# Performance work log

Hardware: AMD Instinct MI355X
Metric: run time of the kernel (lower is better)

Reference implementation:

```python
import jax, jax.numpy as jnp
import numpy as np

N = 50000   # nodes
E = 600000  # edges
D = 128     # in_feats
H = 128     # n_hidden
C = 47      # n_classes


def setup_inputs() -> dict:
    key = jax.random.key(0)
    ks = jax.random.split(key, 12)
    x = jax.random.normal(ks[0], (N, D), dtype=jnp.float32)
    src = jax.random.randint(ks[1], (E,), 0, N, dtype=jnp.int32)
    dst = jax.random.randint(ks[2], (E,), 0, N, dtype=jnp.int32)
    def lin(k, fi, fo):
        s = 1.0 / np.sqrt(fi)
        return jax.random.uniform(k, (fi, fo), jnp.float32, -s, s)
    return {
        "x": x, "src": src, "dst": dst,
        "W_self0": lin(ks[3], D, H), "W_neigh0": lin(ks[4], D, H), "b0": jnp.zeros((H,), jnp.float32),
        "W_self1": lin(ks[5], H, H), "W_neigh1": lin(ks[6], H, H), "b1": jnp.zeros((H,), jnp.float32),
        "W_self2": lin(ks[7], H, C), "W_neigh2": lin(ks[8], H, C), "b2": jnp.zeros((C,), jnp.float32),
    }


def _sage_layer(h, src, dst, W_self, W_neigh, b, act):
    # gather neighbor (src) features, mean-aggregate onto dst nodes
    msum = jax.ops.segment_sum(h[src], dst, num_segments=N)           # [N, F]
    deg = jax.ops.segment_sum(jnp.ones((src.shape[0], 1), h.dtype), dst, num_segments=N)
    h_neigh = msum / jnp.maximum(deg, 1.0)                            # zero-degree -> 0
    out = h @ W_self + h_neigh @ W_neigh + b
    return jax.nn.relu(out) if act else out


def reference(x, src, dst, W_self0, W_neigh0, b0, W_self1, W_neigh1, b1, W_self2, W_neigh2, b2):
    h = _sage_layer(x, src, dst, W_self0, W_neigh0, b0, True)
    h = _sage_layer(h, src, dst, W_self1, W_neigh1, b1, True)
    h = _sage_layer(h, src, dst, W_self2, W_neigh2, b2, False)
    return h
```

## Files before the change

### kernel.cpp

```cpp
#include <hip/hip_runtime.h>
#include <hip/hip_bf16.h>


#define THREADS 256

typedef unsigned short u16;
typedef __attribute__((ext_vector_type(8))) short bf16x8;
typedef __attribute__((ext_vector_type(4))) float f32x4;

__device__ inline u16 f2bf(float f) {
    union { float f; unsigned u; } v; v.f = f;
    unsigned r = (v.u + 0x7FFFu + ((v.u >> 16) & 1u)) >> 16;
    return (u16)r;
}
__device__ inline float bf2f(u16 b) {
    union { unsigned u; float f; } v; v.u = ((unsigned)b) << 16;
    return v.f;
}
__device__ inline unsigned pack2(float a, float b) {
    return (unsigned)f2bf(a) | ((unsigned)f2bf(b) << 16);
}

#define GLDS16(gp, lp)                                                         \
    __builtin_amdgcn_global_load_lds(                                          \
        (const __attribute__((address_space(1))) void*)(gp),                   \
        (__attribute__((address_space(3))) void*)(lp), 16, 0, 0)

__global__ void k_count(const int* __restrict__ dst, int* __restrict__ deg, int E) {
    int e = blockIdx.x * blockDim.x + threadIdx.x;
    if (e < E) atomicAdd(&deg[dst[e]], 1);
}

__global__ void k_scan_block(const int* __restrict__ deg, int* __restrict__ off,
                             int* __restrict__ bsum, int n) {
    __shared__ int s[256];
    int t = threadIdx.x;
    int base = blockIdx.x * 1024 + t * 4;
    int v[4];
#pragma unroll
    for (int i = 0; i < 4; i++) v[i] = (base + i < n) ? deg[base + i] : 0;
    int sum = v[0] + v[1] + v[2] + v[3];
    int val = sum;
    s[t] = val;
    __syncthreads();
    for (int o = 1; o < 256; o <<= 1) {
        int x = (t >= o) ? s[t - o] : 0;
        __syncthreads();
        val += x;
        s[t] = val;
        __syncthreads();
    }
    int run = val - sum;
#pragma unroll
    for (int i = 0; i < 4; i++) {
        if (base + i < n) off[base + i] = run;
        run += v[i];
    }
    if (t == 255) bsum[blockIdx.x] = val;
}

__global__ void k_scan_bsum(int* __restrict__ bsum, int nb) {
    if (threadIdx.x == 0 && blockIdx.x == 0) {
        int acc = 0;
        for (int i = 0; i < nb; i++) { int v = bsum[i]; bsum[i] = acc; acc += v; }
    }
}

__global__ void k_scan_add(int* __restrict__ off, const int* __restrict__ bsum, int n) {
    int t = threadIdx.x;
    int base = blockIdx.x * 1024 + t * 4;
    int add = bsum[blockIdx.x];
#pragma unroll
    for (int i = 0; i < 4; i++)
        if (base + i < n) off[base + i] += add;
}

__global__ void k_fill(const int* __restrict__ src, const int* __restrict__ dst,
                       const int* __restrict__ off, int* __restrict__ cur,
                       int* __restrict__ eidx, int E) {
    int e = blockIdx.x * blockDim.x + threadIdx.x;
    if (e < E) {
        int d = dst[e];
        int p = atomicAdd(&cur[d], 1);
        eidx[off[d] + p] = src[e];
    }
}

__global__ void k_prepX(const float* __restrict__ x, u16* __restrict__ hi,
                        u16* __restrict__ lo, int n32) {
    int i = blockIdx.x * blockDim.x + threadIdx.x;
    if (i >= n32) return;
    float4 v = ((const float4*)x)[i];
    float h0 = bf2f(f2bf(v.x)), h1 = bf2f(f2bf(v.y)), h2 = bf2f(f2bf(v.z)), h3 = bf2f(f2bf(v.w));
    uint2 hp, lp;
    hp.x = pack2(h0, h1); hp.y = pack2(h2, h3);
    lp.x = pack2(v.x - h0, v.y - h1); lp.y = pack2(v.z - h2, v.w - h3);
    ((uint2*)hi)[i] = hp;
    ((uint2*)lo)[i] = lp;
}

__global__ void k_prepW(const float* __restrict__ Ws, const float* __restrict__ Wn,
                        u16* __restrict__ Bthi, u16* __restrict__ Btlo, int fout) {
    int idx = blockIdx.x * blockDim.x + threadIdx.x;
    if (idx >= 128 * 256) return;
    int col = idx >> 8;
    int k = idx & 255;
    float v = 0.f;
    if (col < fout) v = (k < 128) ? Ws[k * fout + col] : Wn[(k - 128) * fout + col];
    u16 h = f2bf(v);
    Bthi[idx] = h;
    Btlo[idx] = f2bf(v - bf2f(h));
}

__global__ void k_aggregate(const u16* __restrict__ hi_in, const int* __restrict__ eidx,
                            const int* __restrict__ off, const int* __restrict__ deg,
                            u16* __restrict__ mhi, u16* __restrict__ mlo, int n) {
    int node = blockIdx.x * 4 + (threadIdx.x >> 6);
    int lane = threadIdx.x & 63;
    if (node >= n) return;
    int cnt = deg[node];
    int base = off[node];
    const unsigned* h1 = (const unsigned*)hi_in;
    float2 acc = make_float2(0.f, 0.f);
    for (int j = 0; j < cnt; j += 8) {
        int s[8];
        float m[8];
#pragma unroll
        for (int u = 0; u < 8; u++) {
            int jj = j + u;
            s[u] = eidx[base + (jj < cnt ? jj : 0)];
            m[u] = (jj < cnt) ? 1.f : 0.f;
        }
        unsigned v[8];
#pragma unroll
        for (int u = 0; u < 8; u++) v[u] = h1[(size_t)s[u] * 64 + lane];
#pragma unroll
        for (int u = 0; u < 8; u++) {
            acc.x = fmaf(m[u], bf2f((u16)(v[u] & 0xffffu)), acc.x);
            acc.y = fmaf(m[u], bf2f((u16)(v[u] >> 16)), acc.y);
        }
    }
    float iv = 1.0f / (float)(cnt > 1 ? cnt : 1);
    float a0 = acc.x * iv, a1 = acc.y * iv;
    float h0 = bf2f(f2bf(a0)), h1v = bf2f(f2bf(a1));
    ((unsigned*)mhi)[(size_t)node * 64 + lane] = pack2(a0, a1);
    ((unsigned*)mlo)[(size_t)node * 64 + lane] = pack2(a0 - h0, a1 - h1v);
}

__global__ __launch_bounds__(256) void k_gemm_mfma(
    const u16* __restrict__ Ahi_s, const u16* __restrict__ Alo_s,
    const u16* __restrict__ Ahi_n, const u16* __restrict__ Alo_n,
    const u16* __restrict__ Bthi, const u16* __restrict__ Btlo,
    const float* __restrict__ bias, float* __restrict__ out_f32,
    u16* __restrict__ out_hi, u16* __restrict__ out_lo, int n, int fout, int relu) {
    __shared__ u16 sAhi[64 * 32];
    __shared__ u16 sAlo[64 * 32];
    __shared__ u16 sBhi[128 * 32];
    __shared__ u16 sBlo[128 * 32];

    int t = threadIdx.x;
    int w = t >> 6;
    int lane = t & 63;
    int wr = w >> 1, wc = w & 1;
    size_t row0 = (size_t)blockIdx.x * 64;

    f32x4 acc[2][4];
#pragma unroll
    for (int r = 0; r < 2; r++)
#pragma unroll
        for (int c = 0; c < 4; c++) acc[r][c] = (f32x4){0.f, 0.f, 0.f, 0.f};

    for (int kk = 0; kk < 256; kk += 32) {
        const u16* Phi = (kk < 128) ? Ahi_s : Ahi_n;
        const u16* Plo = (kk < 128) ? Alo_s : Alo_n;
        int kc = kk & 127;
        __syncthreads();
        {
            int r = w * 16 + (lane >> 2);
            int cb = (lane & 3) * 8;
            GLDS16(Phi + (row0 + r) * 128 + kc + cb, &sAhi[r * 32 + cb]);
            GLDS16(Plo + (row0 + r) * 128 + kc + cb, &sAlo[r * 32 + cb]);
        }
#pragma unroll
        for (int i = 0; i < 2; i++) {
            int c = w * 32 + i * 16 + (lane >> 2);
            int cb = (lane & 3) * 8;
            GLDS16(Bthi + (size_t)c * 256 + kk + cb, &sBhi[c * 32 + cb]);
            GLDS16(Btlo + (size_t)c * 256 + kk + cb, &sBlo[c * 32 + cb]);
        }
        __syncthreads();

        bf16x8 a_hi[2], a_lo[2], b_hi[4], b_lo[4];
        int q8 = (lane >> 4) * 8;
#pragma unroll
        for (int r = 0; r < 2; r++) {
            int ad = (wr * 32 + r * 16 + (lane & 15)) * 32 + q8;
            a_hi[r] = *(const bf16x8*)&sAhi[ad];
            a_lo[r] = *(const bf16x8*)&sAlo[ad];
        }
#pragma unroll
        for (int c = 0; c < 4; c++) {
            int ad = (wc * 64 + c * 16 + (lane & 15)) * 32 + q8;
            b_hi[c] = *(const bf16x8*)&sBhi[ad];
            b_lo[c] = *(const bf16x8*)&sBlo[ad];
        }
#pragma unroll
        for (int r = 0; r < 2; r++)
#pragma unroll
            for (int c = 0; c < 4; c++) {
                acc[r][c] = __builtin_amdgcn_mfma_f32_16x16x32_bf16(
                    a_hi[r], b_hi[c], acc[r][c], 0, 0, 0);
                acc[r][c] = __builtin_amdgcn_mfma_f32_16x16x32_bf16(
                    a_hi[r], b_lo[c], acc[r][c], 0, 0, 0);
                acc[r][c] = __builtin_amdgcn_mfma_f32_16x16x32_bf16(
                    a_lo[r], b_hi[c], acc[r][c], 0, 0, 0);
            }
    }

    int quad = lane >> 4;
    int lcol = lane & 15;
#pragma unroll
    for (int r = 0; r < 2; r++) {
#pragma unroll
        for (int c = 0; c < 4; c++) {
            int col = wc * 64 + c * 16 + lcol;
            float bv = (col < fout) ? bias[col] : 0.f;
#pragma unroll
            for (int g = 0; g < 4; g++) {
                size_t row = row0 + wr * 32 + r * 16 + quad * 4 + g;
                if (row >= (size_t)n || col >= fout) continue;
                float v = acc[r][c][g] + bv;
                if (relu) v = v > 0.f ? v : 0.f;
                if (out_f32) out_f32[row * fout + col] = v;
                if (out_hi) {
                    u16 h = f2bf(v);
                    out_hi[row * 128 + col] = h;
                    out_lo[row * 128 + col] = f2bf(v - bf2f(h));
                }
            }
        }
    }
}

extern "C" void kernel_launch(void* const* d_in, const int* in_sizes, int n_in,
                              void* d_out, int out_size, void* d_ws, size_t ws_size,
                              hipStream_t stream) {
    const float* x = (const float*)d_in[0];
    const int* src = (const int*)d_in[1];
    const int* dst = (const int*)d_in[2];
    const float* Ws0 = (const float*)d_in[3];
    const float* Wn0 = (const float*)d_in[4];
    const float* b0 = (const float*)d_in[5];
    const float* Ws1 = (const float*)d_in[6];
    const float* Wn1 = (const float*)d_in[7];
    const float* b1 = (const float*)d_in[8];
    const float* Ws2 = (const float*)d_in[9];
    const float* Wn2 = (const float*)d_in[10];
    const float* b2 = (const float*)d_in[11];
    float* out = (float*)d_out;

    const int N = in_sizes[0] / 128;
    const int E = in_sizes[1];
    const int Npad = ((N + 63) / 64) * 64;

    char* p = (char*)d_ws;
    u16* P0hi = (u16*)p; p += (size_t)Npad * 128 * 2;
    u16* P0lo = (u16*)p; p += (size_t)Npad * 128 * 2;
    u16* P1hi = (u16*)p; p += (size_t)Npad * 128 * 2;
    u16* P1lo = (u16*)p; p += (size_t)Npad * 128 * 2;
    u16* Mhi = (u16*)p; p += (size_t)Npad * 128 * 2;
    u16* Mlo = (u16*)p; p += (size_t)Npad * 128 * 2;
    u16* Bt0h = (u16*)p; p += 128 * 256 * 2;
    u16* Bt0l = (u16*)p; p += 128 * 256 * 2;
    u16* Bt1h = (u16*)p; p += 128 * 256 * 2;
    u16* Bt1l = (u16*)p; p += 128 * 256 * 2;
    u16* Bt2h = (u16*)p; p += 128 * 256 * 2;
    u16* Bt2l = (u16*)p; p += 128 * 256 * 2;
    int* deg = (int*)p; p += (size_t)N * 4;
    int* off = (int*)p; p += (size_t)N * 4;
    int* cur = (int*)p; p += (size_t)N * 4;
    int* eidx = (int*)p; p += (size_t)E * 4;
    int* bsum = (int*)p;

    const int nbE = (E + THREADS - 1) / THREADS;
    const int nbScan = (N + 1023) / 1024;
    const int nbAgg = (N + 3) / 4;
    const int nbGemm = (N + 63) / 64;
    const int nbPX = (N * 32 + THREADS - 1) / THREADS;
    const int nbPW = (128 * 256 + THREADS - 1) / THREADS;

    hipMemsetAsync(deg, 0, (size_t)N * sizeof(int), stream);
    hipMemsetAsync(cur, 0, (size_t)N * sizeof(int), stream);

    k_count<<<nbE, THREADS, 0, stream>>>(dst, deg, E);
    k_scan_block<<<nbScan, 256, 0, stream>>>(deg, off, bsum, N);
    k_scan_bsum<<<1, 64, 0, stream>>>(bsum, nbScan);
    k_scan_add<<<nbScan, 256, 0, stream>>>(off, bsum, N);
    k_fill<<<nbE, THREADS, 0, stream>>>(src, dst, off, cur, eidx, E);

    k_prepX<<<nbPX, THREADS, 0, stream>>>(x, P0hi, P0lo, N * 32);
    k_prepW<<<nbPW, THREADS, 0, stream>>>(Ws0, Wn0, Bt0h, Bt0l, 128);
    k_prepW<<<nbPW, THREADS, 0, stream>>>(Ws1, Wn1, Bt1h, Bt1l, 128);
    k_prepW<<<nbPW, THREADS, 0, stream>>>(Ws2, Wn2, Bt2h, Bt2l, 47);

    k_aggregate<<<nbAgg, 256, 0, stream>>>(P0hi, eidx, off, deg, Mhi, Mlo, N);
    k_gemm_mfma<<<nbGemm, 256, 0, stream>>>(P0hi, P0lo, Mhi, Mlo, Bt0h, Bt0l, b0,
                                            (float*)nullptr, P1hi, P1lo, N, 128, 1);
    k_aggregate<<<nbAgg, 256, 0, stream>>>(P1hi, eidx, off, deg, Mhi, Mlo, N);
    k_gemm_mfma<<<nbGemm, 256, 0, stream>>>(P1hi, P1lo, Mhi, Mlo, Bt1h, Bt1l, b1,
                                            (float*)nullptr, P0hi, P0lo, N, 128, 1);
    k_aggregate<<<nbAgg, 256, 0, stream>>>(P0hi, eidx, off, deg, Mhi, Mlo, N);
    k_gemm_mfma<<<nbGemm, 256, 0, stream>>>(P0hi, P0lo, Mhi, Mlo, Bt2h, Bt2l, b2,
                                            out, (u16*)nullptr, (u16*)nullptr, N, 47, 0);
}
```

Baseline: 325.5 us.

## Fuse neighbor aggregation into SAGE GEMM kernel via shared-memory staging

Each GEMM block now gathers and mean-aggregates the neighbor features for its 64 rows directly into padded LDS tiles, so the separate aggregate kernel and the Mhi/Mlo round-trip through global memory go away. The gather loop is unrolled to 16 edges. The three weight-prep launches are merged into one, the two memsets into one, and the serial bsum scan is replaced with a wave-shuffle scan. The trade-offs are much larger LDS use per block (about 35 KB extra), which lowers occupancy, and fewer blocks doing the latency-bound gather, so the gather may hide latency less well.

```diff
diff --git a/kernel.cpp b/kernel.cpp
--- a/kernel.cpp
+++ b/kernel.cpp
@@ -60,9 +60,19 @@
 }
 
 __global__ void k_scan_bsum(int* __restrict__ bsum, int nb) {
-    if (threadIdx.x == 0 && blockIdx.x == 0) {
-        int acc = 0;
-        for (int i = 0; i < nb; i++) { int v = bsum[i]; bsum[i] = acc; acc += v; }
+    int lane = threadIdx.x;
+    int carry = 0;
+    for (int start = 0; start < nb; start += 64) {
+        int i = start + lane;
+        int orig = (i < nb) ? bsum[i] : 0;
+        int v = orig;
+#pragma unroll
+        for (int o = 1; o < 64; o <<= 1) {
+            int u = __shfl_up(v, o, 64);
+            if (lane >= o) v += u;
+        }
+        if (i < nb) bsum[i] = carry + v - orig;
+        carry += __shfl(v, 63, 64);
     }
 }
 
@@ -99,60 +109,36 @@
     ((uint2*)lo)[i] = lp;
 }
 
-__global__ void k_prepW(const float* __restrict__ Ws, const float* __restrict__ Wn,
-                        u16* __restrict__ Bthi, u16* __restrict__ Btlo, int fout) {
+__global__ void k_prepW3(const float* __restrict__ Ws0, const float* __restrict__ Wn0,
+                         const float* __restrict__ Ws1, const float* __restrict__ Wn1,
+                         const float* __restrict__ Ws2, const float* __restrict__ Wn2,
+                         u16* __restrict__ Bt) {
     int idx = blockIdx.x * blockDim.x + threadIdx.x;
-    if (idx >= 128 * 256) return;
-    int col = idx >> 8;
-    int k = idx & 255;
+    if (idx >= 3 * 128 * 256) return;
+    int layer = idx >> 15;
+    int within = idx & 32767;
+    int col = within >> 8;
+    int k = within & 255;
+    const float* Ws = (layer == 0) ? Ws0 : (layer == 1) ? Ws1 : Ws2;
+    const float* Wn = (layer == 0) ? Wn0 : (layer == 1) ? Wn1 : Wn2;
+    int fout = (layer == 2) ? 47 : 128;
     float v = 0.f;
     if (col < fout) v = (k < 128) ? Ws[k * fout + col] : Wn[(k - 128) * fout + col];
     u16 h = f2bf(v);
-    Bthi[idx] = h;
-    Btlo[idx] = f2bf(v - bf2f(h));
-}
-
-__global__ void k_aggregate(const u16* __restrict__ hi_in, const int* __restrict__ eidx,
-                            const int* __restrict__ off, const int* __restrict__ deg,
-                            u16* __restrict__ mhi, u16* __restrict__ mlo, int n) {
-    int node = blockIdx.x * 4 + (threadIdx.x >> 6);
-    int lane = threadIdx.x & 63;
-    if (node >= n) return;
-    int cnt = deg[node];
-    int base = off[node];
-    const unsigned* h1 = (const unsigned*)hi_in;
-    float2 acc = make_float2(0.f, 0.f);
-    for (int j = 0; j < cnt; j += 8) {
-        int s[8];
-        float m[8];
-#pragma unroll
-        for (int u = 0; u < 8; u++) {
-            int jj = j + u;
-            s[u] = eidx[base + (jj < cnt ? jj : 0)];
-            m[u] = (jj < cnt) ? 1.f : 0.f;
-        }
-        unsigned v[8];
-#pragma unroll
-        for (int u = 0; u < 8; u++) v[u] = h1[(size_t)s[u] * 64 + lane];
-#pragma unroll
-        for (int u = 0; u < 8; u++) {
-            acc.x = fmaf(m[u], bf2f((u16)(v[u] & 0xffffu)), acc.x);
-            acc.y = fmaf(m[u], bf2f((u16)(v[u] >> 16)), acc.y);
-        }
-    }
-    float iv = 1.0f / (float)(cnt > 1 ? cnt : 1);
-    float a0 = acc.x * iv, a1 = acc.y * iv;
-    float h0 = bf2f(f2bf(a0)), h1v = bf2f(f2bf(a1));
-    ((unsigned*)mhi)[(size_t)node * 64 + lane] = pack2(a0, a1);
-    ((unsigned*)mlo)[(size_t)node * 64 + lane] = pack2(a0 - h0, a1 - h1v);
-}
-
-__global__ __launch_bounds__(256) void k_gemm_mfma(
-    const u16* __restrict__ Ahi_s, const u16* __restrict__ Alo_s,
-    const u16* __restrict__ Ahi_n, const u16* __restrict__ Alo_n,
-    const u16* __restrict__ Bthi, const u16* __restrict__ Btlo,
-    const float* __restrict__ bias, float* __restrict__ out_f32,
-    u16* __restrict__ out_hi, u16* __restrict__ out_lo, int n, int fout, int relu) {
+    Bt[layer * 65536 + within] = h;
+    Bt[layer * 65536 + 32768 + within] = f2bf(v - bf2f(h));
+}
+
+#define NPAD 136
+__global__ __launch_bounds__(256) void k_sage(
+    const u16* __restrict__ Phi, const u16* __restrict__ Plo,
+    const int* __restrict__ eidx, const int* __restrict__ off,
+    const int* __restrict__ deg, const u16* __restrict__ Bthi,
+    const u16* __restrict__ Btlo, const float* __restrict__ bias,
+    float* __restrict__ out_f32, u16* __restrict__ out_hi,
+    u16* __restrict__ out_lo, int n, int fout, int relu) {
+    __shared__ u16 sNh[64 * NPAD];
+    __shared__ u16 sNl[64 * NPAD];
     __shared__ u16 sAhi[64 * 32];
     __shared__ u16 sAlo[64 * 32];
     __shared__ u16 sBhi[128 * 32];
@@ -164,6 +150,47 @@
     int wr = w >> 1, wc = w & 1;
     size_t row0 = (size_t)blockIdx.x * 64;
 
+    {
+        const unsigned* h1 = (const unsigned*)Phi;
+        unsigned* nh32 = (unsigned*)sNh;
+        unsigned* nl32 = (unsigned*)sNl;
+        for (int i = 0; i < 16; i++) {
+            int row = w * 16 + i;
+            size_t node = row0 + row;
+            float a0 = 0.f, a1 = 0.f;
+            if (node < (size_t)n) {
+                int cnt = deg[node];
+                int base = off[node];
+                float2 acc = make_float2(0.f, 0.f);
+                for (int j = 0; j < cnt; j += 16) {
+                    int s[16];
+                    float m[16];
+#pragma unroll
+                    for (int u = 0; u < 16; u++) {
+                        int jj = j + u;
+                        s[u] = eidx[base + (jj < cnt ? jj : 0)];
+                        m[u] = (jj < cnt) ? 1.f : 0.f;
+                    }
+                    unsigned v[16];
+#pragma unroll
+                    for (int u = 0; u < 16; u++) v[u] = h1[(size_t)s[u] * 64 + lane];
+#pragma unroll
+                    for (int u = 0; u < 16; u++) {
+                        acc.x = fmaf(m[u], bf2f((u16)(v[u] & 0xffffu)), acc.x);
+                        acc.y = fmaf(m[u], bf2f((u16)(v[u] >> 16)), acc.y);
+                    }
+                }
+                int cd = deg[node];
+                float iv = 1.0f / (float)(cd > 1 ? cd : 1);
+                a0 = acc.x * iv;
+                a1 = acc.y * iv;
+            }
+            float h0 = bf2f(f2bf(a0)), h1v = bf2f(f2bf(a1));
+            nh32[row * (NPAD / 2) + lane] = pack2(a0, a1);
+            nl32[row * (NPAD / 2) + lane] = pack2(a0 - h0, a1 - h1v);
+        }
+    }
+
     f32x4 acc[2][4];
 #pragma unroll
     for (int r = 0; r < 2; r++)
@@ -171,15 +198,12 @@
         for (int c = 0; c < 4; c++) acc[r][c] = (f32x4){0.f, 0.f, 0.f, 0.f};
 
     for (int kk = 0; kk < 256; kk += 32) {
-        const u16* Phi = (kk < 128) ? Ahi_s : Ahi_n;
-        const u16* Plo = (kk < 128) ? Alo_s : Alo_n;
-        int kc = kk & 127;
         __syncthreads();
-        {
+        if (kk < 128) {
             int r = w * 16 + (lane >> 2);
             int cb = (lane & 3) * 8;
-            GLDS16(Phi + (row0 + r) * 128 + kc + cb, &sAhi[r * 32 + cb]);
-            GLDS16(Plo + (row0 + r) * 128 + kc + cb, &sAlo[r * 32 + cb]);
+            GLDS16(Phi + (row0 + r) * 128 + kk + cb, &sAhi[r * 32 + cb]);
+            GLDS16(Plo + (row0 + r) * 128 + kk + cb, &sAlo[r * 32 + cb]);
         }
 #pragma unroll
         for (int i = 0; i < 2; i++) {
@@ -192,11 +216,21 @@
 
         bf16x8 a_hi[2], a_lo[2], b_hi[4], b_lo[4];
         int q8 = (lane >> 4) * 8;
-#pragma unroll
-        for (int r = 0; r < 2; r++) {
-            int ad = (wr * 32 + r * 16 + (lane & 15)) * 32 + q8;
-            a_hi[r] = *(const bf16x8*)&sAhi[ad];
-            a_lo[r] = *(const bf16x8*)&sAlo[ad];
+        if (kk < 128) {
+#pragma unroll
+            for (int r = 0; r < 2; r++) {
+                int ad = (wr * 32 + r * 16 + (lane & 15)) * 32 + q8;
+                a_hi[r] = *(const bf16x8*)&sAhi[ad];
+                a_lo[r] = *(const bf16x8*)&sAlo[ad];
+            }
+        } else {
+            int kc2 = kk - 128;
+#pragma unroll
+            for (int r = 0; r < 2; r++) {
+                int ad = (wr * 32 + r * 16 + (lane & 15)) * NPAD + kc2 + q8;
+                a_hi[r] = *(const bf16x8*)&sNh[ad];
+                a_lo[r] = *(const bf16x8*)&sNl[ad];
+            }
         }
 #pragma unroll
         for (int c = 0; c < 4; c++) {
@@ -268,29 +302,20 @@
     u16* P0lo = (u16*)p; p += (size_t)Npad * 128 * 2;
     u16* P1hi = (u16*)p; p += (size_t)Npad * 128 * 2;
     u16* P1lo = (u16*)p; p += (size_t)Npad * 128 * 2;
-    u16* Mhi = (u16*)p; p += (size_t)Npad * 128 * 2;
-    u16* Mlo = (u16*)p; p += (size_t)Npad * 128 * 2;
-    u16* Bt0h = (u16*)p; p += 128 * 256 * 2;
-    u16* Bt0l = (u16*)p; p += 128 * 256 * 2;
-    u16* Bt1h = (u16*)p; p += 128 * 256 * 2;
-    u16* Bt1l = (u16*)p; p += 128 * 256 * 2;
-    u16* Bt2h = (u16*)p; p += 128 * 256 * 2;
-    u16* Bt2l = (u16*)p; p += 128 * 256 * 2;
+    u16* Bt = (u16*)p; p += 3 * 2 * 128 * 256 * 2;
     int* deg = (int*)p; p += (size_t)N * 4;
+    int* cur = (int*)p; p += (size_t)N * 4;
     int* off = (int*)p; p += (size_t)N * 4;
-    int* cur = (int*)p; p += (size_t)N * 4;
     int* eidx = (int*)p; p += (size_t)E * 4;
     int* bsum = (int*)p;
 
     const int nbE = (E + THREADS - 1) / THREADS;
     const int nbScan = (N + 1023) / 1024;
-    const int nbAgg = (N + 3) / 4;
     const int nbGemm = (N + 63) / 64;
     const int nbPX = (N * 32 + THREADS - 1) / THREADS;
-    const int nbPW = (128 * 256 + THREADS - 1) / THREADS;
-
-    hipMemsetAsync(deg, 0, (size_t)N * sizeof(int), stream);
-    hipMemsetAsync(cur, 0, (size_t)N * sizeof(int), stream);
+    const int nbPW = (3 * 128 * 256 + THREADS - 1) / THREADS;
+
+    hipMemsetAsync(deg, 0, (size_t)2 * N * sizeof(int), stream);
 
     k_count<<<nbE, THREADS, 0, stream>>>(dst, deg, E);
     k_scan_block<<<nbScan, 256, 0, stream>>>(deg, off, bsum, N);
@@ -299,17 +324,15 @@
     k_fill<<<nbE, THREADS, 0, stream>>>(src, dst, off, cur, eidx, E);
 
     k_prepX<<<nbPX, THREADS, 0, stream>>>(x, P0hi, P0lo, N * 32);
-    k_prepW<<<nbPW, THREADS, 0, stream>>>(Ws0, Wn0, Bt0h, Bt0l, 128);
-    k_prepW<<<nbPW, THREADS, 0, stream>>>(Ws1, Wn1, Bt1h, Bt1l, 128);
-    k_prepW<<<nbPW, THREADS, 0, stream>>>(Ws2, Wn2, Bt2h, Bt2l, 47);
-
-    k_aggregate<<<nbAgg, 256, 0, stream>>>(P0hi, eidx, off, deg, Mhi, Mlo, N);
-    k_gemm_mfma<<<nbGemm, 256, 0, stream>>>(P0hi, P0lo, Mhi, Mlo, Bt0h, Bt0l, b0,
-                                            (float*)nullptr, P1hi, P1lo, N, 128, 1);
-    k_aggregate<<<nbAgg, 256, 0, stream>>>(P1hi, eidx, off, deg, Mhi, Mlo, N);
-    k_gemm_mfma<<<nbGemm, 256, 0, stream>>>(P1hi, P1lo, Mhi, Mlo, Bt1h, Bt1l, b1,
-                                            (float*)nullptr, P0hi, P0lo, N, 128, 1);
-    k_aggregate<<<nbAgg, 256, 0, stream>>>(P0hi, eidx, off, deg, Mhi, Mlo, N);
-    k_gemm_mfma<<<nbGemm, 256, 0, stream>>>(P0hi, P0lo, Mhi, Mlo, Bt2h, Bt2l, b2,
-                                            out, (u16*)nullptr, (u16*)nullptr, N, 47, 0);
-}
+    k_prepW3<<<nbPW, THREADS, 0, stream>>>(Ws0, Wn0, Ws1, Wn1, Ws2, Wn2, Bt);
+
+    k_sage<<<nbGemm, 256, 0, stream>>>(P0hi, P0lo, eidx, off, deg,
+                                       Bt + 0 * 65536, Bt + 0 * 65536 + 32768, b0,
+                                       (float*)nullptr, P1hi, P1lo, N, 128, 1);
+    k_sage<<<nbGemm, 256, 0, stream>>>(P1hi, P1lo, eidx, off, deg,
+                                       Bt + 1 * 65536, Bt + 1 * 65536 + 32768, b1,
+                                       (float*)nullptr, P0hi, P0lo, N, 128, 1);
+    k_sage<<<nbGemm, 256, 0, stream>>>(P0hi, P0lo, eidx, off, deg,
+                                       Bt + 2 * 65536, Bt + 2 * 65536 + 32768, b2,
+                                       out, (u16*)nullptr, (u16*)nullptr, N, 47, 0);
+}
```

Result: slower. 422.4 us (+29.8%).
